# Optimization experiments

Measured on AMD Instinct MI355X. Metric: run time of the kernel, lower is better.

Reference implementation:

```python
import math
import jax, jax.numpy as jnp
import numpy as np

B, N, D, H, PREFIX = 2, 2048, 2048, 16, 512
HD = D // H
ROPE_BASE = 10000.0

def _rope(x):
    # x: [b, h, n, d]; rotate-half RoPE with positions 0..n-1
    d = x.shape[-1]
    n = x.shape[-2]
    inv_freq = 1.0 / (ROPE_BASE ** (jnp.arange(0, d, 2, dtype=jnp.float32) / d))  # [d/2]
    pos = jnp.arange(n, dtype=jnp.float32)
    freqs = pos[:, None] * inv_freq[None, :]            # [n, d/2]
    cos, sin = jnp.cos(freqs), jnp.sin(freqs)
    x1, x2 = x[..., : d // 2], x[..., d // 2 :]
    return jnp.concatenate([x1 * cos - x2 * sin, x2 * cos + x1 * sin], axis=-1).astype(x.dtype)

def setup_inputs() -> dict:
    key = jax.random.key(0)
    ks = jax.random.split(key, 6)
    x = jax.random.normal(ks[0], (B, N, D), dtype=jnp.float32)
    prefix_k = jax.random.normal(ks[1], (B, H, PREFIX, HD), dtype=jnp.float32)
    prefix_v = jax.random.normal(ks[2], (B, H, PREFIX, HD), dtype=jnp.float32)
    Wqkv = jax.random.normal(ks[3], (D, 3 * D), dtype=jnp.float32) * (D ** -0.5)
    bqkv = jnp.zeros((3 * D,), dtype=jnp.float32)
    Wff = jax.random.normal(ks[4], (D, D), dtype=jnp.float32) * (D ** -0.5)
    bff = jnp.zeros((D,), dtype=jnp.float32)
    # causal mask over current tokens; prefix (cache) columns fully visible
    causal = jnp.tril(jnp.ones((N, N), dtype=jnp.int32))
    mask = jnp.concatenate([jnp.ones((N, PREFIX), dtype=jnp.int32), causal], axis=1)[None, None]  # [1,1,N,N+PREFIX]
    return {"x": x, "mask": mask, "prefix_k": prefix_k, "prefix_v": prefix_v,
            "Wqkv": Wqkv, "bqkv": bqkv, "Wff": Wff, "bff": bff}

def reference(x, mask, prefix_k, prefix_v, Wqkv, bqkv, Wff, bff):
    b, n, d = x.shape
    h = prefix_k.shape[1]
    hd = d // h
    qkv = (x @ Wqkv + bqkv).reshape(b, n, 3, h, hd)      # 'b n (c h d)'
    qkv = jnp.transpose(qkv, (2, 0, 3, 1, 4))            # -> c b h n d
    q, k, v = qkv[0], qkv[1], qkv[2]
    k = jnp.concatenate([prefix_k, k], axis=2)           # [b,h,kt,hd]
    v = jnp.concatenate([prefix_v, v], axis=2)
    next_prefix_kv = jnp.stack([k, v])                   # cached BEFORE rope (as in source)
    q = _rope(q)
    k = _rope(k)
    scores = jnp.einsum('bhqd,bhkd->bhqk', q, k) / math.sqrt(hd)
    scores = jnp.where(mask == 0, jnp.finfo(scores.dtype).min, scores)
    probs = jax.nn.softmax(scores, axis=-1)              # dropout_prob=0.0 -> identity
    attn_o = jnp.einsum('bhqk,bhkd->bhqd', probs, v)
    attn_o = jnp.transpose(attn_o, (0, 2, 1, 3)).reshape(b, n, d)
    return attn_o @ Wff + bff, next_prefix_kv
```

## Files before the change

### kernel.cpp

```cpp
#include <hip/hip_runtime.h>
#include <hip/hip_bf16.h>
#include <stdint.h>

#define TPB 256

using f32x4 = __attribute__((ext_vector_type(4))) float;
using s16x8 = __attribute__((ext_vector_type(8))) short;
using s16x4 = __attribute__((ext_vector_type(4))) short;

__device__ __forceinline__ short f2bf(float f){
  union { float f; uint32_t u; } v; v.f = f;
  uint32_t u = v.u;
  uint32_t r = (u + 0x7fffu + ((u >> 16) & 1u)) >> 16;
  return (short)(uint16_t)r;
}
__device__ __forceinline__ float bf2f(short b){
  union { uint32_t u; float f; } v; v.u = ((uint32_t)(uint16_t)b) << 16;
  return v.f;
}
__device__ __forceinline__ f32x4 mfma16(s16x8 a, s16x8 b, f32x4 c){
  return __builtin_amdgcn_mfma_f32_16x16x32_bf16(a, b, c, 0, 0, 0);
}

#define AS1(p) ((const __attribute__((address_space(1))) void*)(p))
#define AS3(p) ((__attribute__((address_space(3))) void*)(p))

__global__ void k_cvt_bf16(const float* __restrict__ src, short* __restrict__ dst, int n8){
  int i = blockIdx.x * TPB + threadIdx.x;
  if (i >= n8) return;
  const float4* s4 = (const float4*)src;
  float4 a = s4[2*i], b = s4[2*i+1];
  s16x8 o;
  o[0]=f2bf(a.x); o[1]=f2bf(a.y); o[2]=f2bf(a.z); o[3]=f2bf(a.w);
  o[4]=f2bf(b.x); o[5]=f2bf(b.y); o[6]=f2bf(b.z); o[7]=f2bf(b.w);
  *(s16x8*)(dst + 8*(size_t)i) = o;
}

__global__ void k_trans_cvt(const float* __restrict__ W, short* __restrict__ WT, int K, int Nn){
  __shared__ float ls[32][33];
  int k0 = blockIdx.x * 32, n0 = blockIdx.y * 32;
  int c = threadIdx.x & 31, i = threadIdx.x >> 5;
#pragma unroll
  for (int rr = 0; rr < 4; rr++){
    int row = i*4 + rr;
    ls[row][c] = W[(size_t)(k0+row)*Nn + n0 + c];
  }
  __syncthreads();
#pragma unroll
  for (int rr = 0; rr < 4; rr++){
    int ro = i*4 + rr;
    WT[(size_t)(n0+ro)*K + k0 + c] = f2bf(ls[c][ro]);
  }
}

template<int EPI>
__global__ void __launch_bounds__(512, 2) k_gemm8(
    const short* __restrict__ A, const short* __restrict__ Bt,
    int Nn, int K,
    const float* __restrict__ bias,
    float* __restrict__ outp,
    float* __restrict__ kvout,
    short* __restrict__ qpre, short* __restrict__ kpre, short* __restrict__ vpre)
{
  __shared__ __align__(16) short As[3][16384];
  __shared__ __align__(16) short Bs[3][8192];
  const int tid = threadIdx.x;
  const int w = tid >> 6, l = tid & 63;
  const int lrow = l & 15, lg = l >> 4;
  const int wm = w >> 1, wn = w & 1;
  const int m0 = blockIdx.x << 8, n0 = blockIdx.y << 7;
  const int NT = K >> 6;

  f32x4 acc[4][4] = {};

#define STAGE_A(slot, t, j) do {                                             \
    int chunk = ((w*4 + (j)) << 6) + l;                                      \
    int row = chunk >> 3, cc = chunk & 7;                                    \
    __builtin_amdgcn_global_load_lds(                                        \
      AS1(A + (size_t)(m0+row)*K + (t)*64 + ((cc ^ (row&7)) << 3)),          \
      AS3(&As[slot][(w*4 + (j)) << 9]), 16, 0, 0);                           \
  } while(0)
#define STAGE_B(slot, t, j) do {                                             \
    int chunk = ((w*2 + (j)) << 6) + l;                                      \
    int row = chunk >> 3, cc = chunk & 7;                                    \
    __builtin_amdgcn_global_load_lds(                                        \
      AS1(Bt + (size_t)(n0+row)*K + (t)*64 + ((cc ^ (row&7)) << 3)),         \
      AS3(&Bs[slot][(w*2 + (j)) << 9]), 16, 0, 0);                           \
  } while(0)

  STAGE_A(0,0,0); STAGE_A(0,0,1); STAGE_A(0,0,2); STAGE_A(0,0,3);
  STAGE_B(0,0,0); STAGE_B(0,0,1);
  STAGE_A(1,1,0); STAGE_A(1,1,1); STAGE_A(1,1,2); STAGE_A(1,1,3);
  STAGE_B(1,1,0); STAGE_B(1,1,1);

  int slot = 0;
  for (int t = 0; t < NT; ++t){
    if (t < NT-1) asm volatile("s_waitcnt vmcnt(6)" ::: "memory");
    else          asm volatile("s_waitcnt vmcnt(0)" ::: "memory");
    __builtin_amdgcn_s_barrier();
    asm volatile("" ::: "memory");
    const int sslot = (slot == 0) ? 2 : slot - 1;
    const bool st = (t+2) < NT;
    const char* ab = (const char*)As[slot];
    const char* bb = (const char*)Bs[slot];

    s16x8 bfr[4][2];
#pragma unroll
    for (int ni = 0; ni < 4; ni++){
      int row = wn*64 + ni*16 + lrow;
#pragma unroll
      for (int ks = 0; ks < 2; ks++)
        bfr[ni][ks] = *(const s16x8*)(bb + row*128 + ((ks*64 + lg*16) ^ ((row&7)<<4)));
    }
    s16x8 af[2][2];
#pragma unroll
    for (int mi = 0; mi < 2; mi++){
      int row = wm*64 + mi*16 + lrow;
#pragma unroll
      for (int ks = 0; ks < 2; ks++)
        af[mi][ks] = *(const s16x8*)(ab + row*128 + ((ks*64 + lg*16) ^ ((row&7)<<4)));
    }
    if (st){ STAGE_A(sslot,t+2,0); STAGE_A(sslot,t+2,1); STAGE_B(sslot,t+2,0); }
    __builtin_amdgcn_s_setprio(1);
#pragma unroll
    for (int ks = 0; ks < 2; ks++)
#pragma unroll
      for (int mi = 0; mi < 2; mi++)
#pragma unroll
        for (int ni = 0; ni < 4; ni++)
          acc[mi][ni] = mfma16(af[mi][ks], bfr[ni][ks], acc[mi][ni]);
    __builtin_amdgcn_s_setprio(0);


    s16x8 af2[2][2];
#pragma unroll
    for (int mi = 0; mi < 2; mi++){
      int row = wm*64 + (mi+2)*16 + lrow;
#pragma unroll
      for (int ks = 0; ks < 2; ks++)
        af2[mi][ks] = *(const s16x8*)(ab + row*128 + ((ks*64 + lg*16) ^ ((row&7)<<4)));
    }
    if (st){ STAGE_A(sslot,t+2,2); STAGE_A(sslot,t+2,3); STAGE_B(sslot,t+2,1); }
    __builtin_amdgcn_s_setprio(1);
#pragma unroll
    for (int ks = 0; ks < 2; ks++)
#pragma unroll
      for (int mi = 0; mi < 2; mi++)
#pragma unroll
        for (int ni = 0; ni < 4; ni++)
          acc[mi+2][ni] = mfma16(af2[mi][ks], bfr[ni][ks], acc[mi+2][ni]);
    __builtin_amdgcn_s_setprio(0);
    slot = (slot == 2) ? 0 : slot + 1;
  }
#undef STAGE_A
#undef STAGE_B

#pragma unroll
  for (int mi = 0; mi < 4; mi++){
#pragma unroll
    for (int ni = 0; ni < 4; ni++){
      const int c  = n0 + wn*64 + ni*16 + lrow;
      const int mb = m0 + wm*64 + mi*16 + lg*4;
      const float bv = bias[c];
      if (EPI == 1){
#pragma unroll
        for (int r = 0; r < 4; r++)
          outp[(size_t)(mb+r)*Nn + c] = acc[mi][ni][r] + bv;
      } else {
        const int s = c >> 11, h = (c >> 7) & 15, tt = c & 127;
#pragma unroll
        for (int r = 0; r < 4; r++){
          const int m = mb + r;
          const int b = m >> 11, n = m & 2047;
          const int bh = b*16 + h;
          const float val = acc[mi][ni][r] + bv;
          if (s == 0){
            qpre[((size_t)bh*2048 + n)*128 + tt] = f2bf(val);
          } else if (s == 1){
            kvout[((size_t)bh*2560 + 512 + n)*128 + tt] = val;
            kpre[((size_t)bh*2048 + n)*128 + tt] = f2bf(val);
          } else {
            kvout[(size_t)(32 + bh)*327680 + (size_t)(512 + n)*128 + tt] = val;
            vpre[((size_t)bh*2048 + n)*128 + tt] = f2bf(val);
          }
        }
      }
    }
  }
}

__global__ void k_rope_k_new(const short* __restrict__ kpre, short* __restrict__ kr){
  int gid = blockIdx.x * TPB + threadIdx.x;
  int jb = (gid & 7) * 8; size_t row = gid >> 3;
  int bh = (int)(row >> 11), n = (int)(row & 2047);
  int pos = 512 + n;
  s16x8 v1 = *(const s16x8*)&kpre[row*128 + jb];
  s16x8 v2 = *(const s16x8*)&kpre[row*128 + 64 + jb];
  s16x8 o1, o2;
#pragma unroll
  for (int e = 0; e < 8; e++){
    float invf = __expf((float)(jb + e) * (-9.210340371976184f/64.0f));
    float sn, cs; __sincosf((float)pos * invf, &sn, &cs);
    float x1 = bf2f(v1[e]), x2 = bf2f(v2[e]);
    o1[e] = f2bf(x1*cs - x2*sn);
    o2[e] = f2bf(x2*cs + x1*sn);
  }
  size_t drow = (size_t)bh*2560 + pos;
  *(s16x8*)&kr[drow*128 + jb]      = o1;
  *(s16x8*)&kr[drow*128 + 64 + jb] = o2;
}

__global__ void k_rope_k_prefix(const float* __restrict__ pk, float* __restrict__ kvout0,
                                short* __restrict__ kr){
  int gid = blockIdx.x * TPB + threadIdx.x;
  int jb = (gid & 7) * 8; size_t row = gid >> 3;
  int bh = (int)(row >> 9), p = (int)(row & 511);
  float4 a1 = *(const float4*)&pk[row*128 + jb];
  float4 a2 = *(const float4*)&pk[row*128 + jb + 4];
  float4 b1 = *(const float4*)&pk[row*128 + 64 + jb];
  float4 b2 = *(const float4*)&pk[row*128 + 64 + jb + 4];
  size_t orow = (size_t)bh*2560 + p;
  *(float4*)&kvout0[orow*128 + jb]          = a1;
  *(float4*)&kvout0[orow*128 + jb + 4]      = a2;
  *(float4*)&kvout0[orow*128 + 64 + jb]     = b1;
  *(float4*)&kvout0[orow*128 + 64 + jb + 4] = b2;
  float x1[8] = {a1.x,a1.y,a1.z,a1.w,a2.x,a2.y,a2.z,a2.w};
  float x2[8] = {b1.x,b1.y,b1.z,b1.w,b2.x,b2.y,b2.z,b2.w};
  s16x8 o1, o2;
#pragma unroll
  for (int e = 0; e < 8; e++){
    float invf = __expf((float)(jb + e) * (-9.210340371976184f/64.0f));
    float sn, cs; __sincosf((float)p * invf, &sn, &cs);
    o1[e] = f2bf(x1[e]*cs - x2[e]*sn);
    o2[e] = f2bf(x2[e]*cs + x1[e]*sn);
  }
  *(s16x8*)&kr[orow*128 + jb]      = o1;
  *(s16x8*)&kr[orow*128 + 64 + jb] = o2;
}

__global__ void k_v_prefix(const float* __restrict__ pv, float* __restrict__ kvout1,
                           short* __restrict__ vT){
  __shared__ float ls[32][129];
  int bh = blockIdx.x >> 4, pt = blockIdx.x & 15;
  int p0 = pt*32, tid = threadIdx.x;
#pragma unroll
  for (int i = 0; i < 16; i++){
    int idx = i*TPB + tid; int p = idx >> 7, t = idx & 127;
    float v = pv[((size_t)bh*512 + p0 + p)*128 + t];
    ls[p][t] = v;
    kvout1[((size_t)bh*2560 + p0 + p)*128 + t] = v;
  }
  __syncthreads();
#pragma unroll
  for (int i = 0; i < 16; i++){
    int idx = i*TPB + tid; int t = idx >> 5, p = idx & 31;
    vT[((size_t)bh*128 + t)*2560 + p0 + p] = f2bf(ls[p][t]);
  }
}

__global__ void k_v_new(const short* __restrict__ vpre, short* __restrict__ vT){
  __shared__ float ls[32][129];
  int bh = blockIdx.x >> 6, nt = blockIdx.x & 63;
  int n0 = nt*32, tid = threadIdx.x;
#pragma unroll
  for (int i = 0; i < 16; i++){
    int idx = i*TPB + tid; int p = idx >> 7, t = idx & 127;
    ls[p][t] = bf2f(vpre[((size_t)bh*2048 + n0 + p)*128 + t]);
  }
  __syncthreads();
#pragma unroll
  for (int i = 0; i < 16; i++){
    int idx = i*TPB + tid; int t = idx >> 5, p = idx & 31;
    vT[((size_t)bh*128 + t)*2560 + 512 + n0 + p] = f2bf(ls[p][t]);
  }
}

__global__ void __launch_bounds__(256, 2) k_attn(
    const short* __restrict__ qr, const short* __restrict__ kr,
    const short* __restrict__ vT, short* __restrict__ attno)
{
  __shared__ short Ks[2][64*128];
  __shared__ short VTs[2][128*64];
  __shared__ short Ps[4][32*64];
  const int bh = blockIdx.x;
  const int qt = 15 - (int)blockIdx.y;
  const int n = 10 + 2*qt;
  const int tid = threadIdx.x, w = tid >> 6, l = tid & 63;
  const int lrow = l & 15, lg = l >> 4;
  const int b = bh >> 4, h = bh & 15;
  const int qbw = qt*128 + w*32;

  s16x8 qf[2][4];
  {
    const float sc = 0.088388347648318447f;
#pragma unroll
    for (int qb = 0; qb < 2; qb++){
      const int nr = qbw + qb*16 + lrow;
      const size_t rr = (size_t)bh*2048 + nr;
#pragma unroll
      for (int ks = 0; ks < 4; ks++)
        qf[qb][ks] = *(const s16x8*)&qr[rr*128 + ks*32 + lg*8];
#pragma unroll
      for (int ks = 0; ks < 2; ks++){
#pragma unroll
        for (int e = 0; e < 8; e++){
          const int j = ks*32 + lg*8 + e;
          const float invf = __expf((float)j * (-9.210340371976184f/64.0f));
          float sn, cs;
          __sincosf((float)nr * invf, &sn, &cs);
          float x1 = bf2f(qf[qb][ks][e]), x2 = bf2f(qf[qb][ks+2][e]);
          qf[qb][ks][e]   = f2bf((x1*cs - x2*sn) * sc);
          qf[qb][ks+2][e] = f2bf((x2*cs + x1*sn) * sc);
        }
      }
    }
  }

#define STAGE_KV(buf, kv0s) do {                                                    \
    _Pragma("unroll")                                                               \
    for (int i_ = 0; i_ < 4; i_++){                                                 \
      int chunk = i_*256 + tid;                                                     \
      int row = chunk >> 4, cc = (chunk & 15) ^ (row & 7);                          \
      __builtin_amdgcn_global_load_lds(                                             \
        AS1(kr + ((size_t)bh*2560 + (kv0s) + row)*128 + cc*8),                      \
        AS3((char*)Ks[buf] + (i_*256 + w*64)*16), 16, 0, 0);                        \
    }                                                                               \
    _Pragma("unroll")                                                               \
    for (int i_ = 0; i_ < 4; i_++){                                                 \
      int chunk = i_*256 + tid;                                                     \
      int row = chunk >> 3, cc = (chunk & 7) ^ (row & 7);                           \
      __builtin_amdgcn_global_load_lds(                                             \
        AS1(vT + ((size_t)bh*128 + row)*2560 + (kv0s) + cc*8),                      \
        AS3((char*)VTs[buf] + (i_*256 + w*64)*16), 16, 0, 0);                       \
    }                                                                               \
  } while(0)

  STAGE_KV(0, 0);
  STAGE_KV(1, 64);

  char* psw = (char*)&Ps[w][0];
  f32x4 acc0[8] = {}, acc1[8] = {};
  float mr0 = -1e30f, ls0 = 0.f;
  float mr1 = -1e30f, ls1 = 0.f;

  for (int t = 0; t < n; t++){
    if (t+1 < n) asm volatile("s_waitcnt vmcnt(8)" ::: "memory");
    else         asm volatile("s_waitcnt vmcnt(0)" ::: "memory");
    __builtin_amdgcn_s_barrier();
    asm volatile("" ::: "memory");
    const char* kb_ = (const char*)Ks[t&1];
    const char* vb_ = (const char*)VTs[t&1];
    const int kv0 = t*64;

    f32x4 sf0[4], sf1[4];
    __builtin_amdgcn_s_setprio(1);
#pragma unroll
    for (int kb = 0; kb < 4; kb++){
      f32x4 s0 = {0.f,0.f,0.f,0.f}, s1 = {0.f,0.f,0.f,0.f};
#pragma unroll
      for (int ks = 0; ks < 4; ks++){
        int row  = kb*16 + lrow;
        int colb = ks*64 + lg*16;
        s16x8 kf = *(const s16x8*)(kb_ + row*256 + (colb ^ ((row&7)<<4)));
        s0 = mfma16(kf, qf[0][ks], s0);
        s1 = mfma16(kf, qf[1][ks], s1);
      }
      sf0[kb] = s0; sf1[kb] = s1;
    }
    __builtin_amdgcn_s_setprio(0);

    if (kv0 + 63 > 512 + qbw){
      const int qme0 = 512 + qbw + lrow;
      const int qme1 = qme0 + 16;
#pragma unroll
      for (int kb = 0; kb < 4; kb++)
#pragma unroll
        for (int r = 0; r < 4; r++){
          int kg = kv0 + kb*16 + lg*4 + r;
          if (kg > qme0) sf0[kb][r] = -1e30f;
          if (kg > qme1) sf1[kb][r] = -1e30f;
        }
    }

    {
      float m_ = fmaxf(
          fmaxf(fmaxf(fmaxf(sf0[0][0],sf0[0][1]),fmaxf(sf0[0][2],sf0[0][3])),
                fmaxf(fmaxf(sf0[1][0],sf0[1][1]),fmaxf(sf0[1][2],sf0[1][3]))),
          fmaxf(fmaxf(fmaxf(sf0[2][0],sf0[2][1]),fmaxf(sf0[2][2],sf0[2][3])),
                fmaxf(fmaxf(sf0[3][0],sf0[3][1]),fmaxf(sf0[3][2],sf0[3][3]))));
      m_ = fmaxf(m_, __shfl_xor(m_, 16));
      m_ = fmaxf(m_, __shfl_xor(m_, 32));
      if (__any(m_ > mr0 + 8.f)){
        float mnew = fmaxf(mr0, m_);
        float sc = __expf(mr0 - mnew);
        mr0 = mnew; ls0 *= sc;
        float scr[4];
#pragma unroll
        for (int r = 0; r < 4; r++)
          scr[r] = __shfl(sc, (l & 48) | (lg*4 + r));
#pragma unroll
        for (int dt = 0; dt < 8; dt++)
#pragma unroll
          for (int r = 0; r < 4; r++) acc0[dt][r] *= scr[r];
      }
#pragma unroll
      for (int kb = 0; kb < 4; kb++){
        float p0 = __expf(sf0[kb][0] - mr0);
        float p1 = __expf(sf0[kb][1] - mr0);
        float p2 = __expf(sf0[kb][2] - mr0);
        float p3 = __expf(sf0[kb][3] - mr0);
        ls0 += (p0+p1)+(p2+p3);
        s16x4 pk4 = { f2bf(p0), f2bf(p1), f2bf(p2), f2bf(p3) };
        *(s16x4*)(psw + (lrow*128 + ((kb*32 + lg*8) ^ ((lrow&7)<<4)))) = pk4;
      }
    }
    {
      float m_ = fmaxf(
          fmaxf(fmaxf(fmaxf(sf1[0][0],sf1[0][1]),fmaxf(sf1[0][2],sf1[0][3])),
                fmaxf(fmaxf(sf1[1][0],sf1[1][1]),fmaxf(sf1[1][2],sf1[1][3]))),
          fmaxf(fmaxf(fmaxf(sf1[2][0],sf1[2][1]),fmaxf(sf1[2][2],sf1[2][3])),
                fmaxf(fmaxf(sf1[3][0],sf1[3][1]),fmaxf(sf1[3][2],sf1[3][3]))));
      m_ = fmaxf(m_, __shfl_xor(m_, 16));
      m_ = fmaxf(m_, __shfl_xor(m_, 32));
      if (__any(m_ > mr1 + 8.f)){
        float mnew = fmaxf(mr1, m_);
        float sc = __expf(mr1 - mnew);
        mr1 = mnew; ls1 *= sc;
        float scr[4];
#pragma unroll
        for (int r = 0; r < 4; r++)
          scr[r] = __shfl(sc, (l & 48) | (lg*4 + r));
#pragma unroll
        for (int dt = 0; dt < 8; dt++)
#pragma unroll
          for (int r = 0; r < 4; r++) acc1[dt][r] *= scr[r];
      }
#pragma unroll
      for (int kb = 0; kb < 4; kb++){
        float p0 = __expf(sf1[kb][0] - mr1);
        float p1 = __expf(sf1[kb][1] - mr1);
        float p2 = __expf(sf1[kb][2] - mr1);
        float p3 = __expf(sf1[kb][3] - mr1);
        ls1 += (p0+p1)+(p2+p3);
        s16x4 pk4 = { f2bf(p0), f2bf(p1), f2bf(p2), f2bf(p3) };
        *(s16x4*)(psw + ((16 + lrow)*128 + ((kb*32 + lg*8) ^ ((lrow&7)<<4)))) = pk4;
      }
    }

    __builtin_amdgcn_s_setprio(1);
#pragma unroll
    for (int kp = 0; kp < 2; kp++){
      s16x8 pa0 = *(const s16x8*)(psw + (lrow*128       + ((kp*64 + lg*16) ^ ((lrow&7)<<4))));
      s16x8 pa1 = *(const s16x8*)(psw + ((16+lrow)*128  + ((kp*64 + lg*16) ^ ((lrow&7)<<4))));
#pragma unroll
      for (int dt = 0; dt < 8; dt++){
        int vrow = dt*16 + lrow;
        int vcolb = kp*64 + lg*16;
        s16x8 vf = *(const s16x8*)(vb_ + vrow*128 + (vcolb ^ ((vrow&7)<<4)));
        acc0[dt] = mfma16(pa0, vf, acc0[dt]);
        acc1[dt] = mfma16(pa1, vf, acc1[dt]);
      }
    }
    __builtin_amdgcn_s_setprio(0);

    asm volatile("" ::: "memory");
    __builtin_amdgcn_s_barrier();
    asm volatile("" ::: "memory");
    if (t + 2 < n) STAGE_KV(t&1, (t+2)*64);
  }

  float lsa = ls0;
  lsa += __shfl_xor(lsa, 16);
  lsa += __shfl_xor(lsa, 32);
  float lsb = ls1;
  lsb += __shfl_xor(lsb, 16);
  lsb += __shfl_xor(lsb, 32);
  float linv0[4], linv1[4];
#pragma unroll
  for (int r = 0; r < 4; r++){
    linv0[r] = 1.f / __shfl(lsa, (l & 48) | (lg*4 + r));
    linv1[r] = 1.f / __shfl(lsb, (l & 48) | (lg*4 + r));
  }
#pragma unroll
  for (int dt = 0; dt < 8; dt++){
#pragma unroll
    for (int r = 0; r < 4; r++){
      const int dcol = h*128 + dt*16 + lrow;
      const int nrow0 = qbw + lg*4 + r;
      const int nrow1 = qbw + 16 + lg*4 + r;
      attno[((size_t)b*2048 + nrow0)*2048 + dcol] = f2bf(acc0[dt][r] * linv0[r]);
      attno[((size_t)b*2048 + nrow1)*2048 + dcol] = f2bf(acc1[dt][r] * linv1[r]);
    }
  }
#undef STAGE_KV
}

extern "C" void kernel_launch(void* const* d_in, const int* in_sizes, int n_in,
                              void* d_out, int out_size, void* d_ws, size_t ws_size,
                              hipStream_t stream)
{
  const float* x    = (const float*)d_in[0];
  const float* pk   = (const float*)d_in[2];
  const float* pv   = (const float*)d_in[3];
  const float* Wqkv = (const float*)d_in[4];
  const float* bqkv = (const float*)d_in[5];
  const float* Wff  = (const float*)d_in[6];
  const float* bff  = (const float*)d_in[7];
  float* out   = (float*)d_out;
  float* kvout = out + 8388608;

  char* ws = (char*)d_ws;
  short* xb    = (short*)(ws);
  short* wqkvT = (short*)(ws + 16777216);
  short* wffT  = (short*)(ws + 41943040);
  short* qpre  = (short*)(ws + 50331648);
  short* kpre  = (short*)(ws + 67108864);
  short* vpre  = (short*)(ws + 83886080);
  short* krp   = (short*)(ws + 117440512);
  short* vTp   = (short*)(ws + 138412032);
  short* attno = (short*)(ws + 159383552);

  k_cvt_bf16<<<4096, TPB, 0, stream>>>(x, xb, 1048576);
  k_trans_cvt<<<dim3(64, 192), TPB, 0, stream>>>(Wqkv, wqkvT, 2048, 6144);
  k_trans_cvt<<<dim3(64, 64),  TPB, 0, stream>>>(Wff,  wffT,  2048, 2048);

  k_gemm8<0><<<dim3(16, 48), 512, 0, stream>>>(xb, wqkvT, 6144, 2048, bqkv,
                                               nullptr, kvout, qpre, kpre, vpre);

  k_rope_k_new<<<2048, TPB, 0, stream>>>(kpre, krp);
  k_rope_k_prefix<<<512, TPB, 0, stream>>>(pk, kvout, krp);
  k_v_prefix<<<512, TPB, 0, stream>>>(pv, kvout + (size_t)32*327680, vTp);
  k_v_new<<<2048, TPB, 0, stream>>>(vpre, vTp);

  k_attn<<<dim3(32, 16), 256, 0, stream>>>(qpre, krp, vTp, attno);

  k_gemm8<1><<<dim3(16, 16), 512, 0, stream>>>(attno, wffT, 2048, 2048, bff,
                                               out, nullptr, nullptr, nullptr, nullptr);
}
```

Measured before the change: 305.8 us.

## Merge prep kernels, use exp2 softmax, and stage attention output through LDS

Four small rope/transposition kernels become two launches, each picking its branch by block index, which cuts launch overhead. The attention softmax now folds log2(e) into the Q scale and uses the native exp2 instruction instead of __expf. The lazy-rescale threshold is raised to match the base-2 domain. The attention output is written to shared memory first and then stored to global as coalesced 16-byte rows instead of scattered 2-byte stores. The shared-memory staging adds a block barrier and reuses the K buffer.

Measured after the change: 302.4 us. Within noise of the previous version (-1.1%).

```diff
diff --git a/kernel.cpp b/kernel.cpp
--- a/kernel.cpp
+++ b/kernel.cpp
@@ -131,7 +131,6 @@
           acc[mi][ni] = mfma16(af[mi][ks], bfr[ni][ks], acc[mi][ni]);
     __builtin_amdgcn_s_setprio(0);
 
-
     s16x8 af2[2][2];
 #pragma unroll
     for (int mi = 0; mi < 2; mi++){
@@ -189,89 +188,95 @@
   }
 }
 
-__global__ void k_rope_k_new(const short* __restrict__ kpre, short* __restrict__ kr){
-  int gid = blockIdx.x * TPB + threadIdx.x;
-  int jb = (gid & 7) * 8; size_t row = gid >> 3;
-  int bh = (int)(row >> 11), n = (int)(row & 2047);
-  int pos = 512 + n;
-  s16x8 v1 = *(const s16x8*)&kpre[row*128 + jb];
-  s16x8 v2 = *(const s16x8*)&kpre[row*128 + 64 + jb];
-  s16x8 o1, o2;
-#pragma unroll
-  for (int e = 0; e < 8; e++){
-    float invf = __expf((float)(jb + e) * (-9.210340371976184f/64.0f));
-    float sn, cs; __sincosf((float)pos * invf, &sn, &cs);
-    float x1 = bf2f(v1[e]), x2 = bf2f(v2[e]);
-    o1[e] = f2bf(x1*cs - x2*sn);
-    o2[e] = f2bf(x2*cs + x1*sn);
-  }
-  size_t drow = (size_t)bh*2560 + pos;
-  *(s16x8*)&kr[drow*128 + jb]      = o1;
-  *(s16x8*)&kr[drow*128 + 64 + jb] = o2;
-}
-
-__global__ void k_rope_k_prefix(const float* __restrict__ pk, float* __restrict__ kvout0,
-                                short* __restrict__ kr){
-  int gid = blockIdx.x * TPB + threadIdx.x;
-  int jb = (gid & 7) * 8; size_t row = gid >> 3;
-  int bh = (int)(row >> 9), p = (int)(row & 511);
-  float4 a1 = *(const float4*)&pk[row*128 + jb];
-  float4 a2 = *(const float4*)&pk[row*128 + jb + 4];
-  float4 b1 = *(const float4*)&pk[row*128 + 64 + jb];
-  float4 b2 = *(const float4*)&pk[row*128 + 64 + jb + 4];
-  size_t orow = (size_t)bh*2560 + p;
-  *(float4*)&kvout0[orow*128 + jb]          = a1;
-  *(float4*)&kvout0[orow*128 + jb + 4]      = a2;
-  *(float4*)&kvout0[orow*128 + 64 + jb]     = b1;
-  *(float4*)&kvout0[orow*128 + 64 + jb + 4] = b2;
-  float x1[8] = {a1.x,a1.y,a1.z,a1.w,a2.x,a2.y,a2.z,a2.w};
-  float x2[8] = {b1.x,b1.y,b1.z,b1.w,b2.x,b2.y,b2.z,b2.w};
-  s16x8 o1, o2;
-#pragma unroll
-  for (int e = 0; e < 8; e++){
-    float invf = __expf((float)(jb + e) * (-9.210340371976184f/64.0f));
-    float sn, cs; __sincosf((float)p * invf, &sn, &cs);
-    o1[e] = f2bf(x1[e]*cs - x2[e]*sn);
-    o2[e] = f2bf(x2[e]*cs + x1[e]*sn);
-  }
-  *(s16x8*)&kr[orow*128 + jb]      = o1;
-  *(s16x8*)&kr[orow*128 + 64 + jb] = o2;
-}
-
-__global__ void k_v_prefix(const float* __restrict__ pv, float* __restrict__ kvout1,
-                           short* __restrict__ vT){
+__global__ void k_pre_new(const short* __restrict__ kpre, short* __restrict__ kr,
+                          const short* __restrict__ vpre, short* __restrict__ vT){
   __shared__ float ls[32][129];
-  int bh = blockIdx.x >> 4, pt = blockIdx.x & 15;
-  int p0 = pt*32, tid = threadIdx.x;
-#pragma unroll
-  for (int i = 0; i < 16; i++){
-    int idx = i*TPB + tid; int p = idx >> 7, t = idx & 127;
-    float v = pv[((size_t)bh*512 + p0 + p)*128 + t];
-    ls[p][t] = v;
-    kvout1[((size_t)bh*2560 + p0 + p)*128 + t] = v;
-  }
-  __syncthreads();
-#pragma unroll
-  for (int i = 0; i < 16; i++){
-    int idx = i*TPB + tid; int t = idx >> 5, p = idx & 31;
-    vT[((size_t)bh*128 + t)*2560 + p0 + p] = f2bf(ls[p][t]);
-  }
-}
-
-__global__ void k_v_new(const short* __restrict__ vpre, short* __restrict__ vT){
+  const int tid = threadIdx.x;
+  if (blockIdx.x < 2048){
+    int gid = blockIdx.x * TPB + tid;
+    int jb = (gid & 7) * 8; size_t row = gid >> 3;
+    int bh = (int)(row >> 11), n = (int)(row & 2047);
+    int pos = 512 + n;
+    s16x8 v1 = *(const s16x8*)&kpre[row*128 + jb];
+    s16x8 v2 = *(const s16x8*)&kpre[row*128 + 64 + jb];
+    s16x8 o1, o2;
+#pragma unroll
+    for (int e = 0; e < 8; e++){
+      float invf = __expf((float)(jb + e) * (-9.210340371976184f/64.0f));
+      float sn, cs; __sincosf((float)pos * invf, &sn, &cs);
+      float x1 = bf2f(v1[e]), x2 = bf2f(v2[e]);
+      o1[e] = f2bf(x1*cs - x2*sn);
+      o2[e] = f2bf(x2*cs + x1*sn);
+    }
+    size_t drow = (size_t)bh*2560 + pos;
+    *(s16x8*)&kr[drow*128 + jb]      = o1;
+    *(s16x8*)&kr[drow*128 + 64 + jb] = o2;
+  } else {
+    int bid = (int)blockIdx.x - 2048;
+    int bh = bid >> 6, nt = bid & 63;
+    int n0 = nt*32;
+#pragma unroll
+    for (int i = 0; i < 16; i++){
+      int idx = i*TPB + tid; int p = idx >> 7, t = idx & 127;
+      ls[p][t] = bf2f(vpre[((size_t)bh*2048 + n0 + p)*128 + t]);
+    }
+    __syncthreads();
+#pragma unroll
+    for (int i = 0; i < 16; i++){
+      int idx = i*TPB + tid; int t = idx >> 5, p = idx & 31;
+      vT[((size_t)bh*128 + t)*2560 + 512 + n0 + p] = f2bf(ls[p][t]);
+    }
+  }
+}
+
+__global__ void k_pre_prefix(const float* __restrict__ pk, float* __restrict__ kvout0,
+                             short* __restrict__ kr,
+                             const float* __restrict__ pv, float* __restrict__ kvout1,
+                             short* __restrict__ vT){
   __shared__ float ls[32][129];
-  int bh = blockIdx.x >> 6, nt = blockIdx.x & 63;
-  int n0 = nt*32, tid = threadIdx.x;
-#pragma unroll
-  for (int i = 0; i < 16; i++){
-    int idx = i*TPB + tid; int p = idx >> 7, t = idx & 127;
-    ls[p][t] = bf2f(vpre[((size_t)bh*2048 + n0 + p)*128 + t]);
-  }
-  __syncthreads();
-#pragma unroll
-  for (int i = 0; i < 16; i++){
-    int idx = i*TPB + tid; int t = idx >> 5, p = idx & 31;
-    vT[((size_t)bh*128 + t)*2560 + 512 + n0 + p] = f2bf(ls[p][t]);
+  const int tid = threadIdx.x;
+  if (blockIdx.x < 512){
+    int gid = (int)blockIdx.x * TPB + tid;
+    int jb = (gid & 7) * 8; size_t row = gid >> 3;
+    int bh = (int)(row >> 9), p = (int)(row & 511);
+    float4 a1 = *(const float4*)&pk[row*128 + jb];
+    float4 a2 = *(const float4*)&pk[row*128 + jb + 4];
+    float4 b1 = *(const float4*)&pk[row*128 + 64 + jb];
+    float4 b2 = *(const float4*)&pk[row*128 + 64 + jb + 4];
+    size_t orow = (size_t)bh*2560 + p;
+    *(float4*)&kvout0[orow*128 + jb]          = a1;
+    *(float4*)&kvout0[orow*128 + jb + 4]      = a2;
+    *(float4*)&kvout0[orow*128 + 64 + jb]     = b1;
+    *(float4*)&kvout0[orow*128 + 64 + jb + 4] = b2;
+    float x1[8] = {a1.x,a1.y,a1.z,a1.w,a2.x,a2.y,a2.z,a2.w};
+    float x2[8] = {b1.x,b1.y,b1.z,b1.w,b2.x,b2.y,b2.z,b2.w};
+    s16x8 o1, o2;
+#pragma unroll
+    for (int e = 0; e < 8; e++){
+      float invf = __expf((float)(jb + e) * (-9.210340371976184f/64.0f));
+      float sn, cs; __sincosf((float)p * invf, &sn, &cs);
+      o1[e] = f2bf(x1[e]*cs - x2[e]*sn);
+      o2[e] = f2bf(x2[e]*cs + x1[e]*sn);
+    }
+    *(s16x8*)&kr[orow*128 + jb]      = o1;
+    *(s16x8*)&kr[orow*128 + 64 + jb] = o2;
+  } else {
+    int bid = (int)blockIdx.x - 512;
+    int bh = bid >> 4, pt = bid & 15;
+    int p0 = pt*32;
+#pragma unroll
+    for (int i = 0; i < 16; i++){
+      int idx = i*TPB + tid; int p = idx >> 7, t = idx & 127;
+      float v = pv[((size_t)bh*512 + p0 + p)*128 + t];
+      ls[p][t] = v;
+      kvout1[((size_t)bh*2560 + p0 + p)*128 + t] = v;
+    }
+    __syncthreads();
+#pragma unroll
+    for (int i = 0; i < 16; i++){
+      int idx = i*TPB + tid; int t = idx >> 5, p = idx & 31;
+      vT[((size_t)bh*128 + t)*2560 + p0 + p] = f2bf(ls[p][t]);
+    }
   }
 }
 
@@ -292,7 +297,7 @@
 
   s16x8 qf[2][4];
   {
-    const float sc = 0.088388347648318447f;
+    const float sc = 0.088388347648318447f * 1.4426950408889634f;
 #pragma unroll
     for (int qb = 0; qb < 2; qb++){
       const int nr = qbw + qb*16 + lrow;
@@ -390,9 +395,9 @@
                 fmaxf(fmaxf(sf0[3][0],sf0[3][1]),fmaxf(sf0[3][2],sf0[3][3]))));
       m_ = fmaxf(m_, __shfl_xor(m_, 16));
       m_ = fmaxf(m_, __shfl_xor(m_, 32));
-      if (__any(m_ > mr0 + 8.f)){
+      if (__any(m_ > mr0 + 11.5f)){
         float mnew = fmaxf(mr0, m_);
-        float sc = __expf(mr0 - mnew);
+        float sc = __builtin_amdgcn_exp2f(mr0 - mnew);
         mr0 = mnew; ls0 *= sc;
         float scr[4];
 #pragma unroll
@@ -405,10 +410,10 @@
       }
 #pragma unroll
       for (int kb = 0; kb < 4; kb++){
-        float p0 = __expf(sf0[kb][0] - mr0);
-        float p1 = __expf(sf0[kb][1] - mr0);
-        float p2 = __expf(sf0[kb][2] - mr0);
-        float p3 = __expf(sf0[kb][3] - mr0);
+        float p0 = __builtin_amdgcn_exp2f(sf0[kb][0] - mr0);
+        float p1 = __builtin_amdgcn_exp2f(sf0[kb][1] - mr0);
+        float p2 = __builtin_amdgcn_exp2f(sf0[kb][2] - mr0);
+        float p3 = __builtin_amdgcn_exp2f(sf0[kb][3] - mr0);
         ls0 += (p0+p1)+(p2+p3);
         s16x4 pk4 = { f2bf(p0), f2bf(p1), f2bf(p2), f2bf(p3) };
         *(s16x4*)(psw + (lrow*128 + ((kb*32 + lg*8) ^ ((lrow&7)<<4)))) = pk4;
@@ -422,9 +427,9 @@
                 fmaxf(fmaxf(sf1[3][0],sf1[3][1]),fmaxf(sf1[3][2],sf1[3][3]))));
       m_ = fmaxf(m_, __shfl_xor(m_, 16));
       m_ = fmaxf(m_, __shfl_xor(m_, 32));
-      if (__any(m_ > mr1 + 8.f)){
+      if (__any(m_ > mr1 + 11.5f)){
         float mnew = fmaxf(mr1, m_);
-        float sc = __expf(mr1 - mnew);
+        float sc = __builtin_amdgcn_exp2f(mr1 - mnew);
         mr1 = mnew; ls1 *= sc;
         float scr[4];
 #pragma unroll
@@ -437,10 +442,10 @@
       }
 #pragma unroll
       for (int kb = 0; kb < 4; kb++){
-        float p0 = __expf(sf1[kb][0] - mr1);
-        float p1 = __expf(sf1[kb][1] - mr1);
-        float p2 = __expf(sf1[kb][2] - mr1);
-        float p3 = __expf(sf1[kb][3] - mr1);
+        float p0 = __builtin_amdgcn_exp2f(sf1[kb][0] - mr1);
+        float p1 = __builtin_amdgcn_exp2f(sf1[kb][1] - mr1);
+        float p2 = __builtin_amdgcn_exp2f(sf1[kb][2] - mr1);
+        float p3 = __builtin_amdgcn_exp2f(sf1[kb][3] - mr1);
         ls1 += (p0+p1)+(p2+p3);
         s16x4 pk4 = { f2bf(p0), f2bf(p1), f2bf(p2), f2bf(p3) };
         *(s16x4*)(psw + ((16 + lrow)*128 + ((kb*32 + lg*8) ^ ((lrow&7)<<4)))) = pk4;
@@ -481,16 +486,24 @@
     linv0[r] = 1.f / __shfl(lsa, (l & 48) | (lg*4 + r));
     linv1[r] = 1.f / __shfl(lsb, (l & 48) | (lg*4 + r));
   }
+  short* lout = (short*)Ks;
 #pragma unroll
   for (int dt = 0; dt < 8; dt++){
 #pragma unroll
     for (int r = 0; r < 4; r++){
-      const int dcol = h*128 + dt*16 + lrow;
-      const int nrow0 = qbw + lg*4 + r;
-      const int nrow1 = qbw + 16 + lg*4 + r;
-      attno[((size_t)b*2048 + nrow0)*2048 + dcol] = f2bf(acc0[dt][r] * linv0[r]);
-      attno[((size_t)b*2048 + nrow1)*2048 + dcol] = f2bf(acc1[dt][r] * linv1[r]);
-    }
+      const int col = dt*16 + lrow;
+      lout[(w*32 + lg*4 + r)*128 + col]      = f2bf(acc0[dt][r] * linv0[r]);
+      lout[(w*32 + 16 + lg*4 + r)*128 + col] = f2bf(acc1[dt][r] * linv1[r]);
+    }
+  }
+  __syncthreads();
+  const size_t gbase = ((size_t)b*2048 + qt*128)*2048 + (size_t)h*128;
+#pragma unroll
+  for (int i = 0; i < 8; i++){
+    const int row = (tid >> 4) + i*16;
+    const int chunk = tid & 15;
+    s16x8 v = *(const s16x8*)&lout[row*128 + chunk*8];
+    *(s16x8*)&attno[gbase + (size_t)row*2048 + chunk*8] = v;
   }
 #undef STAGE_KV
 }
@@ -527,10 +540,9 @@
   k_gemm8<0><<<dim3(16, 48), 512, 0, stream>>>(xb, wqkvT, 6144, 2048, bqkv,
                                                nullptr, kvout, qpre, kpre, vpre);
 
-  k_rope_k_new<<<2048, TPB, 0, stream>>>(kpre, krp);
-  k_rope_k_prefix<<<512, TPB, 0, stream>>>(pk, kvout, krp);
-  k_v_prefix<<<512, TPB, 0, stream>>>(pv, kvout + (size_t)32*327680, vTp);
-  k_v_new<<<2048, TPB, 0, stream>>>(vpre, vTp);
+  k_pre_new<<<4096, TPB, 0, stream>>>(kpre, krp, vpre, vTp);
+  k_pre_prefix<<<1024, TPB, 0, stream>>>(pk, kvout, krp,
+                                         pv, kvout + (size_t)32*327680, vTp);
 
   k_attn<<<dim3(32, 16), 256, 0, stream>>>(qpre, krp, vTp, attno);
 
```
